# Kernel optimization log

Measured on AMD Instinct MI355X. Metric: run time of the kernel, lower is better.

The kernel has to match this reference:

```python
import jax, jax.numpy as jnp
import numpy as np

B, T, D = 16, 2048, 256
WINDOW = 128


def setup_inputs() -> dict:
    key = jax.random.key(0)
    ks = jax.random.split(key, 6)
    scale = 1.0 / np.sqrt(D)
    return {
        "x": jax.random.normal(ks[0], (B, T, D), dtype=jnp.float32),
        "Wq": jax.random.normal(ks[1], (D, D), dtype=jnp.float32) * scale,
        "Wk": jax.random.normal(ks[2], (D, D), dtype=jnp.float32) * scale,
        "Wv": jax.random.normal(ks[3], (D, D), dtype=jnp.float32) * scale,
        "Wo": jax.random.normal(ks[4], (D, D), dtype=jnp.float32) * scale,
        "w_bias": jax.random.normal(ks[5], (T, T), dtype=jnp.float32) * 0.1,
        "window": WINDOW,
    }


def reference(x, Wq, Wk, Wv, Wo, w_bias, window):
    # x: [B,T,D]; w_bias: [T,T] learned pairwise position bias.
    T_ = x.shape[1]
    q = jnp.einsum("btd,de->bte", x, Wq)
    k = jnp.einsum("btd,de->bte", x, Wk)
    v = jnp.einsum("btd,de->bte", x, Wv)

    # AFT-Local: bias is zeroed outside the local band |t - t'| < window,
    # but ALL positions still contribute (with bias 0) to the weighted sum.
    idx = jnp.arange(T_)
    band = jnp.abs(idx[:, None] - idx[None, :]) < window  # [T,T] bool
    w_local = jnp.where(band, w_bias, 0.0)

    # Stable exponentials: the num/den ratio is invariant to per-row shifts
    # of w and per-(b,d) shifts of k.
    w_stable = w_local - jnp.max(w_local, axis=1, keepdims=True)
    k_stable = k - jnp.max(k, axis=1, keepdims=True)
    expw = jnp.exp(w_stable)  # [T,T]
    expk = jnp.exp(k_stable)  # [B,T,D]

    num = jnp.einsum("ts,bsd->btd", expw, expk * v)
    den = jnp.einsum("ts,bsd->btd", expw, expk)
    y = jax.nn.sigmoid(q) * (num / den)
    return jnp.einsum("btd,de->bte", y, Wo)
```

## Files before the change

### kernel.cpp

```cpp
#include <hip/hip_runtime.h>
#include <math.h>

#define B_ 16
#define T_ 2048
#define D_ 256
#define W_ 128
#define M_ (B_*T_)

typedef __attribute__((ext_vector_type(8))) short bf16x8;
typedef __attribute__((ext_vector_type(4))) float f32x4;
typedef unsigned short u16;

static __device__ __forceinline__ u16 f32_bf16_rne(float f) {
    unsigned int u = __float_as_uint(f);
    u += 0x7FFF + ((u >> 16) & 1);
    return (u16)(u >> 16);
}
static __device__ __forceinline__ float bf16_f32(u16 h) {
    return __uint_as_float(((unsigned int)h) << 16);
}

__global__ __launch_bounds__(256) void aft_split_wT(
    const float* __restrict__ Wq, const float* __restrict__ Wk,
    const float* __restrict__ Wv, const float* __restrict__ Wo,
    u16* __restrict__ Wth, u16* __restrict__ Wkl)
{
    const float* Ws[4] = {Wq, Wk, Wv, Wo};
    const float* W = Ws[blockIdx.x];
    const int n  = blockIdx.y * 16 + (threadIdx.x >> 4);
    const int k0 = (threadIdx.x & 15) * 16;
    size_t obase = ((size_t)blockIdx.x * 256 + n) * 256 + k0;
    #pragma unroll 4
    for (int j = 0; j < 16; ++j) {
        float v = W[(size_t)(k0 + j) * 256 + n];
        u16 h = f32_bf16_rne(v);
        Wth[obase + j] = h;
        if (blockIdx.x == 1)
            Wkl[(size_t)n * 256 + k0 + j] = f32_bf16_rne(v - bf16_f32(h));
    }
}

__global__ void aft_ewb(const float* __restrict__ wb, u16* __restrict__ EWb)
{
    const int t = blockIdx.x;
    const int j = threadIdx.x;
    const int s = (t & ~63) - 128 + j;
    const int dlt = s - t;
    float v = 0.f;
    if (s >= 0 && s < T_ && dlt > -W_ && dlt < W_)
        v = expf(wb[(size_t)t * T_ + s]) - 1.0f;
    EWb[(size_t)t * 320 + j] = f32_bf16_rne(v);
}

__global__ __launch_bounds__(256) void aft_qkv_mfma(
    const float* __restrict__ x,
    const u16* __restrict__ Wth, const u16* __restrict__ Wkl,
    u16* __restrict__ ekT, u16* __restrict__ sigqT)
{
    __shared__ alignas(16) u16 sm[20480];
    u16* Ah = sm;
    u16* Al = sm + 5120;
    u16* Bs = sm + 10240;
    u16* Tr = sm;

    const int tid  = threadIdx.x;
    const int row0 = blockIdx.x * 128;
    const int col0 = blockIdx.y * 64;
    const int b    = row0 >> 11;
    const int t0g  = row0 & (T_ - 1);
    const int lane = tid & 63;
    const int wid  = tid >> 6;
    const int wm   = (wid & 1) * 64;
    const int wn   = (wid >> 1) * 32;
    const int qd   = lane >> 4;
    const int r    = lane & 15;

    f32x4 accq[4][2], acck[4][2], accv[4][2];
    #pragma unroll
    for (int i = 0; i < 4; ++i)
        #pragma unroll
        for (int j = 0; j < 2; ++j) {
            accq[i][j] = (f32x4){0.f, 0.f, 0.f, 0.f};
            acck[i][j] = accq[i][j];
            accv[i][j] = accq[i][j];
        }

    const int am   = tid >> 1;
    const int akh  = (tid & 1) * 16;
    const int brow = tid >> 2;
    const int bseg = (tid & 3) * 8;

    for (int k0 = 0; k0 < D_; k0 += 32) {
        {
            size_t g = (size_t)(row0 + am) * D_ + k0 + akh;
            union { ushort4 s4[4]; u16 h[16]; } H, L;
            #pragma unroll
            for (int c = 0; c < 4; ++c) {
                float4 v = *(const float4*)&x[g + c * 4];
                float vv[4] = {v.x, v.y, v.z, v.w};
                #pragma unroll
                for (int e = 0; e < 4; ++e) {
                    u16 h = f32_bf16_rne(vv[e]);
                    H.h[c * 4 + e] = h;
                    L.h[c * 4 + e] = f32_bf16_rne(vv[e] - bf16_f32(h));
                }
            }
            *(ushort4*)&Ah[am * 40 + akh]      = H.s4[0];
            *(ushort4*)&Ah[am * 40 + akh + 4]  = H.s4[1];
            *(ushort4*)&Ah[am * 40 + akh + 8]  = H.s4[2];
            *(ushort4*)&Ah[am * 40 + akh + 12] = H.s4[3];
            *(ushort4*)&Al[am * 40 + akh]      = L.s4[0];
            *(ushort4*)&Al[am * 40 + akh + 4]  = L.s4[1];
            *(ushort4*)&Al[am * 40 + akh + 8]  = L.s4[2];
            *(ushort4*)&Al[am * 40 + akh + 12] = L.s4[3];
        }
        {
            size_t nrow = (size_t)(col0 + brow) * 256 + k0 + bseg;
            uint4 vq  = *(const uint4*)&Wth[nrow];
            uint4 vkh = *(const uint4*)&Wth[65536 + nrow];
            uint4 vkl = *(const uint4*)&Wkl[nrow];
            uint4 vv  = *(const uint4*)&Wth[2 * 65536 + nrow];
            *(uint4*)&Bs[0 * 2560 + brow * 40 + bseg] = vq;
            *(uint4*)&Bs[1 * 2560 + brow * 40 + bseg] = vkh;
            *(uint4*)&Bs[2 * 2560 + brow * 40 + bseg] = vkl;
            *(uint4*)&Bs[3 * 2560 + brow * 40 + bseg] = vv;
        }
        __syncthreads();

        bf16x8 ah[4], al[4];
        #pragma unroll
        for (int mf = 0; mf < 4; ++mf) {
            ah[mf] = *(const bf16x8*)&Ah[(wm + mf * 16 + r) * 40 + qd * 8];
            al[mf] = *(const bf16x8*)&Al[(wm + mf * 16 + r) * 40 + qd * 8];
        }
        #pragma unroll
        for (int nf = 0; nf < 2; ++nf) {
            int br = (wn + nf * 16 + r) * 40 + qd * 8;
            bf16x8 bq  = *(const bf16x8*)&Bs[br];
            bf16x8 bkh = *(const bf16x8*)&Bs[2560 + br];
            bf16x8 bkl = *(const bf16x8*)&Bs[5120 + br];
            bf16x8 bv  = *(const bf16x8*)&Bs[7680 + br];
            #pragma unroll
            for (int mf = 0; mf < 4; ++mf) {
                accq[mf][nf] = __builtin_amdgcn_mfma_f32_16x16x32_bf16(ah[mf], bq,  accq[mf][nf], 0, 0, 0);
                acck[mf][nf] = __builtin_amdgcn_mfma_f32_16x16x32_bf16(ah[mf], bkh, acck[mf][nf], 0, 0, 0);
                acck[mf][nf] = __builtin_amdgcn_mfma_f32_16x16x32_bf16(ah[mf], bkl, acck[mf][nf], 0, 0, 0);
                acck[mf][nf] = __builtin_amdgcn_mfma_f32_16x16x32_bf16(al[mf], bkh, acck[mf][nf], 0, 0, 0);
                accv[mf][nf] = __builtin_amdgcn_mfma_f32_16x16x32_bf16(ah[mf], bv,  accv[mf][nf], 0, 0, 0);
            }
        }
        __syncthreads();
    }

    const int dl_r = tid >> 2;
    const int tseg = (tid & 3) * 32;
    #pragma unroll
    for (int round = 0; round < 3; ++round) {
        __syncthreads();
        #pragma unroll
        for (int mf = 0; mf < 4; ++mf) {
            #pragma unroll
            for (int nf = 0; nf < 2; ++nf) {
                ushort4 o;
                float vals[4];
                #pragma unroll
                for (int reg = 0; reg < 4; ++reg) {
                    if (round == 0)      vals[reg] = expf(acck[mf][nf][reg]);
                    else if (round == 1) vals[reg] = expf(acck[mf][nf][reg]) * accv[mf][nf][reg];
                    else                 vals[reg] = 1.f / (1.f + expf(-accq[mf][nf][reg]));
                }
                o.x = f32_bf16_rne(vals[0]); o.y = f32_bf16_rne(vals[1]);
                o.z = f32_bf16_rne(vals[2]); o.w = f32_bf16_rne(vals[3]);
                int dl = wn + nf * 16 + r;
                int tt = wm + mf * 16 + qd * 4;
                *(ushort4*)&Tr[dl * 136 + tt] = o;
            }
        }
        __syncthreads();
        u16* dst;
        if (round == 0)      dst = ekT   + ((size_t)(b * 512 + col0 + dl_r)) * 2048;
        else if (round == 1) dst = ekT   + ((size_t)(b * 512 + 256 + col0 + dl_r)) * 2048;
        else                 dst = sigqT + ((size_t)(b * 256 + col0 + dl_r)) * 2048;
        dst += t0g + tseg;
        const u16* srcp = &Tr[dl_r * 136 + tseg];
        #pragma unroll
        for (int i = 0; i < 4; ++i)
            *(uint4*)&dst[i * 8] = *(const uint4*)&srcp[i * 8];
    }
}

__global__ __launch_bounds__(256) void aft_sums(
    const u16* __restrict__ ekT, float* __restrict__ Sk, float* __restrict__ Sv)
{
    const int wid  = threadIdx.x >> 6;
    const int lane = threadIdx.x & 63;
    const int row  = blockIdx.x * 4 + wid;
    const int b = row >> 9, n = row & 511;
    const u16* p = ekT + (size_t)row * 2048 + lane * 32;
    float s = 0.f;
    #pragma unroll
    for (int c = 0; c < 4; ++c) {
        union { uint4 v; u16 h[8]; } u;
        u.v = *(const uint4*)&p[c * 8];
        #pragma unroll
        for (int i = 0; i < 8; ++i) s += bf16_f32(u.h[i]);
    }
    #pragma unroll
    for (int off = 32; off >= 1; off >>= 1) s += __shfl_down(s, off, 64);
    if (lane == 0) {
        if (n < 256) Sk[b * 256 + n] = s;
        else         Sv[b * 256 + n - 256] = s;
    }
}

__global__ __launch_bounds__(256) void aft_band_mfma(
    const u16* __restrict__ EWb, const u16* __restrict__ ekT,
    const u16* __restrict__ sigqT,
    const float* __restrict__ Sk, const float* __restrict__ Sv,
    u16* __restrict__ yTD)
{
    __shared__ alignas(16) u16 sm[12800];
    u16* Aw  = sm;
    u16* Bkv = sm + 2560;

    const int tid  = threadIdx.x;
    const int t0   = blockIdx.x * 64;
    const int b    = blockIdx.y >> 1;
    const int dh   = (blockIdx.y & 1) * 128;
    const int lane = tid & 63;
    const int wid  = tid >> 6;
    const int wn   = wid * 32;
    const int qd   = lane >> 4;
    const int r    = lane & 15;

    f32x4 accn[4][2], accd[4][2];
    #pragma unroll
    for (int i = 0; i < 4; ++i)
        #pragma unroll
        for (int j = 0; j < 2; ++j) {
            accn[i][j] = (f32x4){0.f, 0.f, 0.f, 0.f};
            accd[i][j] = (f32x4){0.f, 0.f, 0.f, 0.f};
        }

    const int atl = tid >> 2;
    const int ak8 = (tid & 3) * 8;

    for (int c = 0; c < 10; ++c) {
        const int sc = t0 - 128 + c * 32;
        if (sc < 0 || sc >= T_) continue;
        __syncthreads();
        *(uint4*)&Aw[atl * 40 + ak8] =
            *(const uint4*)&EWb[(size_t)(t0 + atl) * 320 + c * 32 + ak8];
        #pragma unroll
        for (int rr = 0; rr < 4; ++rr) {
            int nl = rr * 64 + atl;
            int n  = (nl < 128) ? (dh + nl) : (256 + dh + nl - 128);
            *(uint4*)&Bkv[nl * 40 + ak8] =
                *(const uint4*)&ekT[((size_t)(b * 512) + n) * 2048 + sc + ak8];
        }
        __syncthreads();

        bf16x8 af[4];
        #pragma unroll
        for (int mf = 0; mf < 4; ++mf)
            af[mf] = *(const bf16x8*)&Aw[(mf * 16 + r) * 40 + qd * 8];
        #pragma unroll
        for (int nf = 0; nf < 2; ++nf) {
            bf16x8 be = *(const bf16x8*)&Bkv[(wn + nf * 16 + r) * 40 + qd * 8];
            bf16x8 bv = *(const bf16x8*)&Bkv[(128 + wn + nf * 16 + r) * 40 + qd * 8];
            #pragma unroll
            for (int mf = 0; mf < 4; ++mf) {
                accd[mf][nf] = __builtin_amdgcn_mfma_f32_16x16x32_bf16(af[mf], be, accd[mf][nf], 0, 0, 0);
                accn[mf][nf] = __builtin_amdgcn_mfma_f32_16x16x32_bf16(af[mf], bv, accn[mf][nf], 0, 0, 0);
            }
        }
    }

    __syncthreads();
    u16* Ly = sm;
    #pragma unroll
    for (int nf = 0; nf < 2; ++nf) {
        const int dl = wn + nf * 16 + r;
        const int d  = dh + dl;
        const float skq = Sk[(b << 8) + d];
        const float svq = Sv[(b << 8) + d];
        #pragma unroll
        for (int mf = 0; mf < 4; ++mf) {
            const int tt = t0 + mf * 16 + qd * 4;
            size_t off = ((size_t)(b << 8) + d) * 2048 + tt;
            ushort4 sg = *(const ushort4*)&sigqT[off];
            float s4[4] = {bf16_f32(sg.x), bf16_f32(sg.y), bf16_f32(sg.z), bf16_f32(sg.w)};
            #pragma unroll
            for (int reg = 0; reg < 4; ++reg) {
                float y = s4[reg] * (svq + accn[mf][nf][reg]) / (skq + accd[mf][nf][reg]);
                Ly[(mf * 16 + qd * 4 + reg) * 136 + dl] = f32_bf16_rne(y);
            }
        }
    }
    __syncthreads();
    {
        const int tl  = tid >> 2;
        const int ds4 = (tid & 3) * 32;
        u16* dst = yTD + ((size_t)b * 2048 + t0 + tl) * 256 + dh + ds4;
        #pragma unroll
        for (int i = 0; i < 4; ++i)
            *(uint4*)&dst[i * 8] = *(const uint4*)&Ly[tl * 136 + ds4 + i * 8];
    }
}

__global__ __launch_bounds__(256) void aft_out_mfma(
    const u16* __restrict__ yTD, const u16* __restrict__ Woth,
    float* __restrict__ out)
{
    __shared__ alignas(16) u16 sm[7680];
    u16* As = sm;
    u16* Bh = sm + 2560;

    const int tid  = threadIdx.x;
    const int row0 = blockIdx.x * 64;
    const int col0 = blockIdx.y * 128;
    const int lane = tid & 63;
    const int wid  = tid >> 6;
    const int wn   = wid * 32;
    const int qd   = lane >> 4;
    const int r    = lane & 15;

    f32x4 acc[4][2];
    #pragma unroll
    for (int i = 0; i < 4; ++i)
        #pragma unroll
        for (int j = 0; j < 2; ++j)
            acc[i][j] = (f32x4){0.f, 0.f, 0.f, 0.f};

    const int arow = tid >> 2;
    const int aseg = (tid & 3) * 8;
    const int brw  = tid >> 1;
    const int bsg  = (tid & 1) * 16;

    for (int k0 = 0; k0 < D_; k0 += 32) {
        {
            uint4 v = *(const uint4*)&yTD[(size_t)(row0 + arow) * 256 + k0 + aseg];
            *(uint4*)&As[arow * 40 + aseg] = v;
        }
        {
            size_t g = (size_t)(col0 + brw) * 256 + k0 + bsg;
            uint4 v0 = *(const uint4*)&Woth[g];
            uint4 v1 = *(const uint4*)&Woth[g + 8];
            *(uint4*)&Bh[brw * 40 + bsg]     = v0;
            *(uint4*)&Bh[brw * 40 + bsg + 8] = v1;
        }
        __syncthreads();

        bf16x8 af[4];
        #pragma unroll
        for (int mf = 0; mf < 4; ++mf)
            af[mf] = *(const bf16x8*)&As[(mf * 16 + r) * 40 + qd * 8];
        #pragma unroll
        for (int nf = 0; nf < 2; ++nf) {
            bf16x8 bh = *(const bf16x8*)&Bh[(wn + nf * 16 + r) * 40 + qd * 8];
            #pragma unroll
            for (int mf = 0; mf < 4; ++mf)
                acc[mf][nf] = __builtin_amdgcn_mfma_f32_16x16x32_bf16(af[mf], bh, acc[mf][nf], 0, 0, 0);
        }
        __syncthreads();
    }

    #pragma unroll
    for (int mf = 0; mf < 4; ++mf)
        #pragma unroll
        for (int nf = 0; nf < 2; ++nf)
            #pragma unroll
            for (int reg = 0; reg < 4; ++reg) {
                int mrow = row0 + mf * 16 + qd * 4 + reg;
                int ncol = col0 + wn + nf * 16 + r;
                out[(size_t)mrow * D_ + ncol] = acc[mf][nf][reg];
            }
}

extern "C" void kernel_launch(void* const* d_in, const int* in_sizes, int n_in,
                              void* d_out, int out_size, void* d_ws, size_t ws_size,
                              hipStream_t stream)
{
    const float* x  = (const float*)d_in[0];
    const float* Wq = (const float*)d_in[1];
    const float* Wk = (const float*)d_in[2];
    const float* Wv = (const float*)d_in[3];
    const float* Wo = (const float*)d_in[4];
    const float* wb = (const float*)d_in[5];

    u16* Wth   = (u16*)d_ws;
    u16* Wkl   = Wth + 262144;
    u16* EWb   = Wkl + 65536;
    u16* ekT   = EWb + 655360;
    u16* sigqT = ekT + 16777216;
    u16* yTD   = sigqT + 8388608;
    float* Sk  = (float*)(yTD + 8388608);
    float* Sv  = Sk + 4096;

    aft_split_wT<<<dim3(4, 16), 256, 0, stream>>>(Wq, Wk, Wv, Wo, Wth, Wkl);
    aft_ewb<<<dim3(T_), 320, 0, stream>>>(wb, EWb);
    aft_qkv_mfma<<<dim3(M_ / 128, 4), 256, 0, stream>>>(x, Wth, Wkl, ekT, sigqT);
    aft_sums<<<dim3(8192 / 4), 256, 0, stream>>>(ekT, Sk, Sv);
    aft_band_mfma<<<dim3(T_ / 64, B_ * 2), 256, 0, stream>>>(EWb, ekT, sigqT, Sk, Sv, yTD);
    aft_out_mfma<<<dim3(M_ / 64, 2), 256, 0, stream>>>(yTD, Wth + 3 * 65536, (float*)d_out);
}
```

Measured before the change: 201.8 us.

## Pre-split x to bf16 hi/lo and load MFMA operands directly from global

Adds a separate kernel that converts x into bf16 high and low halves once, and the QKV GEMM then reads A and B fragments straight from global memory, dropping shared-memory staging and the per-k-step barriers. The weight transpose-split kernel now goes through a shared-memory tile so its reads and writes are coalesced. The extra pass writes and rereads x at bf16 width, reusing the yTD buffer and extra workspace, and relies on cache hits because the direct global fragment loads are no longer shared across the block.

```diff
diff --git a/kernel.cpp b/kernel.cpp
--- a/kernel.cpp
+++ b/kernel.cpp
@@ -25,18 +25,39 @@
     const float* __restrict__ Wv, const float* __restrict__ Wo,
     u16* __restrict__ Wth, u16* __restrict__ Wkl)
 {
+    __shared__ alignas(16) u16 Th[64][72];
+    __shared__ alignas(16) u16 Tl[64][72];
     const float* Ws[4] = {Wq, Wk, Wv, Wo};
-    const float* W = Ws[blockIdx.x];
-    const int n  = blockIdx.y * 16 + (threadIdx.x >> 4);
-    const int k0 = (threadIdx.x & 15) * 16;
-    size_t obase = ((size_t)blockIdx.x * 256 + n) * 256 + k0;
-    #pragma unroll 4
-    for (int j = 0; j < 16; ++j) {
-        float v = W[(size_t)(k0 + j) * 256 + n];
-        u16 h = f32_bf16_rne(v);
-        Wth[obase + j] = h;
-        if (blockIdx.x == 1)
-            Wkl[(size_t)n * 256 + k0 + j] = f32_bf16_rne(v - bf16_f32(h));
+    const int mat = blockIdx.x;
+    const float* W = Ws[mat];
+    const int k0 = (blockIdx.y & 3) * 64;
+    const int n0 = (blockIdx.y >> 2) * 64;
+    const int tid = threadIdx.x;
+
+    #pragma unroll
+    for (int p = 0; p < 4; ++p) {
+        const int k = p * 16 + (tid >> 4);
+        const int n = (tid & 15) * 4;
+        float4 v = *(const float4*)&W[(size_t)(k0 + k) * 256 + n0 + n];
+        float vv[4] = {v.x, v.y, v.z, v.w};
+        #pragma unroll
+        for (int e = 0; e < 4; ++e) {
+            u16 h = f32_bf16_rne(vv[e]);
+            Th[n + e][k] = h;
+            Tl[n + e][k] = f32_bf16_rne(vv[e] - bf16_f32(h));
+        }
+    }
+    __syncthreads();
+
+    const int n  = tid >> 2;
+    const int kc = (tid & 3) * 16;
+    size_t ob = ((size_t)mat * 256 + n0 + n) * 256 + k0 + kc;
+    *(uint4*)&Wth[ob]     = *(const uint4*)&Th[n][kc];
+    *(uint4*)&Wth[ob + 8] = *(const uint4*)&Th[n][kc + 8];
+    if (mat == 1) {
+        size_t ol = ((size_t)(n0 + n)) * 256 + k0 + kc;
+        *(uint4*)&Wkl[ol]     = *(const uint4*)&Tl[n][kc];
+        *(uint4*)&Wkl[ol + 8] = *(const uint4*)&Tl[n][kc + 8];
     }
 }
 
@@ -52,15 +73,32 @@
     EWb[(size_t)t * 320 + j] = f32_bf16_rne(v);
 }
 
+__global__ __launch_bounds__(256) void aft_xsplit(
+    const float* __restrict__ x, u16* __restrict__ xh, u16* __restrict__ xl)
+{
+    const size_t i0 = ((size_t)blockIdx.x * 256 + threadIdx.x) * 8;
+    union { uint4 v; u16 h[8]; } H, L;
+    #pragma unroll
+    for (int c = 0; c < 2; ++c) {
+        float4 v = *(const float4*)&x[i0 + c * 4];
+        float vv[4] = {v.x, v.y, v.z, v.w};
+        #pragma unroll
+        for (int e = 0; e < 4; ++e) {
+            u16 h = f32_bf16_rne(vv[e]);
+            H.h[c * 4 + e] = h;
+            L.h[c * 4 + e] = f32_bf16_rne(vv[e] - bf16_f32(h));
+        }
+    }
+    *(uint4*)&xh[i0] = H.v;
+    *(uint4*)&xl[i0] = L.v;
+}
+
 __global__ __launch_bounds__(256) void aft_qkv_mfma(
-    const float* __restrict__ x,
+    const u16* __restrict__ xh, const u16* __restrict__ xl,
     const u16* __restrict__ Wth, const u16* __restrict__ Wkl,
     u16* __restrict__ ekT, u16* __restrict__ sigqT)
 {
-    __shared__ alignas(16) u16 sm[20480];
-    u16* Ah = sm;
-    u16* Al = sm + 5120;
-    u16* Bs = sm + 10240;
+    __shared__ alignas(16) u16 sm[8704];
     u16* Tr = sm;
 
     const int tid  = threadIdx.x;
@@ -85,61 +123,29 @@
             accv[i][j] = accq[i][j];
         }
 
-    const int am   = tid >> 1;
-    const int akh  = (tid & 1) * 16;
-    const int brow = tid >> 2;
-    const int bseg = (tid & 3) * 8;
+    size_t aro[4];
+    #pragma unroll
+    for (int mf = 0; mf < 4; ++mf)
+        aro[mf] = (size_t)(row0 + wm + mf * 16 + r) * 256 + qd * 8;
+    size_t cro[2];
+    #pragma unroll
+    for (int nf = 0; nf < 2; ++nf)
+        cro[nf] = (size_t)(col0 + wn + nf * 16 + r) * 256 + qd * 8;
 
     for (int k0 = 0; k0 < D_; k0 += 32) {
-        {
-            size_t g = (size_t)(row0 + am) * D_ + k0 + akh;
-            union { ushort4 s4[4]; u16 h[16]; } H, L;
-            #pragma unroll
-            for (int c = 0; c < 4; ++c) {
-                float4 v = *(const float4*)&x[g + c * 4];
-                float vv[4] = {v.x, v.y, v.z, v.w};
-                #pragma unroll
-                for (int e = 0; e < 4; ++e) {
-                    u16 h = f32_bf16_rne(vv[e]);
-                    H.h[c * 4 + e] = h;
-                    L.h[c * 4 + e] = f32_bf16_rne(vv[e] - bf16_f32(h));
-                }
-            }
-            *(ushort4*)&Ah[am * 40 + akh]      = H.s4[0];
-            *(ushort4*)&Ah[am * 40 + akh + 4]  = H.s4[1];
-            *(ushort4*)&Ah[am * 40 + akh + 8]  = H.s4[2];
-            *(ushort4*)&Ah[am * 40 + akh + 12] = H.s4[3];
-            *(ushort4*)&Al[am * 40 + akh]      = L.s4[0];
-            *(ushort4*)&Al[am * 40 + akh + 4]  = L.s4[1];
-            *(ushort4*)&Al[am * 40 + akh + 8]  = L.s4[2];
-            *(ushort4*)&Al[am * 40 + akh + 12] = L.s4[3];
-        }
-        {
-            size_t nrow = (size_t)(col0 + brow) * 256 + k0 + bseg;
-            uint4 vq  = *(const uint4*)&Wth[nrow];
-            uint4 vkh = *(const uint4*)&Wth[65536 + nrow];
-            uint4 vkl = *(const uint4*)&Wkl[nrow];
-            uint4 vv  = *(const uint4*)&Wth[2 * 65536 + nrow];
-            *(uint4*)&Bs[0 * 2560 + brow * 40 + bseg] = vq;
-            *(uint4*)&Bs[1 * 2560 + brow * 40 + bseg] = vkh;
-            *(uint4*)&Bs[2 * 2560 + brow * 40 + bseg] = vkl;
-            *(uint4*)&Bs[3 * 2560 + brow * 40 + bseg] = vv;
-        }
-        __syncthreads();
-
         bf16x8 ah[4], al[4];
         #pragma unroll
         for (int mf = 0; mf < 4; ++mf) {
-            ah[mf] = *(const bf16x8*)&Ah[(wm + mf * 16 + r) * 40 + qd * 8];
-            al[mf] = *(const bf16x8*)&Al[(wm + mf * 16 + r) * 40 + qd * 8];
+            ah[mf] = *(const bf16x8*)&xh[aro[mf] + k0];
+            al[mf] = *(const bf16x8*)&xl[aro[mf] + k0];
         }
         #pragma unroll
         for (int nf = 0; nf < 2; ++nf) {
-            int br = (wn + nf * 16 + r) * 40 + qd * 8;
-            bf16x8 bq  = *(const bf16x8*)&Bs[br];
-            bf16x8 bkh = *(const bf16x8*)&Bs[2560 + br];
-            bf16x8 bkl = *(const bf16x8*)&Bs[5120 + br];
-            bf16x8 bv  = *(const bf16x8*)&Bs[7680 + br];
+            const size_t co = cro[nf] + k0;
+            bf16x8 bq  = *(const bf16x8*)&Wth[co];
+            bf16x8 bkh = *(const bf16x8*)&Wth[65536 + co];
+            bf16x8 bkl = *(const bf16x8*)&Wkl[co];
+            bf16x8 bv  = *(const bf16x8*)&Wth[2 * 65536 + co];
             #pragma unroll
             for (int mf = 0; mf < 4; ++mf) {
                 accq[mf][nf] = __builtin_amdgcn_mfma_f32_16x16x32_bf16(ah[mf], bq,  accq[mf][nf], 0, 0, 0);
@@ -149,7 +155,6 @@
                 accv[mf][nf] = __builtin_amdgcn_mfma_f32_16x16x32_bf16(ah[mf], bv,  accv[mf][nf], 0, 0, 0);
             }
         }
-        __syncthreads();
     }
 
     const int dl_r = tid >> 2;
@@ -396,10 +401,13 @@
     u16* yTD   = sigqT + 8388608;
     float* Sk  = (float*)(yTD + 8388608);
     float* Sv  = Sk + 4096;
+    u16* xl    = (u16*)(Sv + 4096);
+    u16* xh    = yTD;
 
     aft_split_wT<<<dim3(4, 16), 256, 0, stream>>>(Wq, Wk, Wv, Wo, Wth, Wkl);
     aft_ewb<<<dim3(T_), 320, 0, stream>>>(wb, EWb);
-    aft_qkv_mfma<<<dim3(M_ / 128, 4), 256, 0, stream>>>(x, Wth, Wkl, ekT, sigqT);
+    aft_xsplit<<<dim3(M_ * D_ / (256 * 8)), 256, 0, stream>>>(x, xh, xl);
+    aft_qkv_mfma<<<dim3(M_ / 128, 4), 256, 0, stream>>>(xh, xl, Wth, Wkl, ekT, sigqT);
     aft_sums<<<dim3(8192 / 4), 256, 0, stream>>>(ekT, Sk, Sv);
     aft_band_mfma<<<dim3(T_ / 64, B_ * 2), 256, 0, stream>>>(EWb, ekT, sigqT, Sk, Sv, yTD);
     aft_out_mfma<<<dim3(M_ / 64, 2), 256, 0, stream>>>(yTD, Wth + 3 * 65536, (float*)d_out);
```

Result: slower. 240.9 us (+19.4%).
